# Kernel tuning notes

Measured on AMD Instinct MI355X. Metric: run time of the kernel, lower is better.

The kernel has to match this reference:

```python
import jax, jax.numpy as jnp
from jax import lax
import numpy as np

# ---- static config derived from init_kwargs ----
BATCH, SEQ, DM = 16, 1024, 512
EXPAND, DSTATE, DCONV, HEADDIM = 2, 64, 4, 64
DIN = EXPAND * DM                 # 1024 (d_inner)
NH = DIN // HEADDIM               # 16 heads
CONVDIM = DIN + 2 * DSTATE        # 1152 (x, B, C share depthwise conv)
DINPROJ = 2 * DIN + 2 * DSTATE + NH  # 2192
IN_CH, OUT_CH = SEQ, 1024         # Conv1d sees (B, L, d_model) as (N, C=L, len=d_model)
EPS = 1e-5


def setup_inputs() -> dict:
    key = jax.random.key(0)
    ks = jax.random.split(key, 8)
    sc = lambda k, shape, s=0.02: jax.random.normal(k, shape, jnp.float32) * s
    return {
        "x": jax.random.normal(ks[0], (BATCH, SEQ, DM), jnp.float32),
        # Mamba2 params (bias=False for in/out proj by default)
        "in_proj_w": sc(ks[1], (DINPROJ, DM)),
        "conv1d_w": sc(ks[2], (CONVDIM, DCONV), 0.1),   # depthwise kernel
        "conv1d_b": jnp.zeros((CONVDIM,), jnp.float32),
        "dt_bias": sc(ks[3], (NH,), 0.1),
        "A_log": jnp.log(jnp.linspace(1.0, 16.0, NH, dtype=jnp.float32)),
        "D": jnp.ones((NH,), jnp.float32),
        "rms_w": jnp.ones((DIN,), jnp.float32),
        "out_proj_w": sc(ks[4], (DM, DIN)),
        # trailing Conv1d(in_channels=SEQ, out_channels, k=3, pad=1)
        "conv_w": sc(ks[5], (OUT_CH, IN_CH, 3)),
        "conv_b": jnp.zeros((OUT_CH,), jnp.float32),
        # BatchNorm1d affine params (training-mode batch stats)
        "bn_gamma": jnp.ones((OUT_CH,), jnp.float32),
        "bn_beta": jnp.zeros((OUT_CH,), jnp.float32),
    }


def _mamba2(u, in_proj_w, conv1d_w, conv1d_b, dt_bias, A_log, D, rms_w, out_proj_w):
    B, L, _ = u.shape
    zxbcdt = u @ in_proj_w.T                          # (B, L, DINPROJ)
    z = zxbcdt[..., :DIN]
    xBC = zxbcdt[..., DIN:DIN + CONVDIM]
    dt = zxbcdt[..., DIN + CONVDIM:]                  # (B, L, NH)
    dt = jax.nn.softplus(dt + dt_bias)

    # causal depthwise conv over time + SiLU
    xBC_t = jnp.pad(xBC.transpose(0, 2, 1), ((0, 0), (0, 0), (DCONV - 1, 0)))
    xBC_c = lax.conv_general_dilated(
        xBC_t, conv1d_w[:, None, :], (1,), 'VALID',
        dimension_numbers=('NCH', 'OIH', 'NCH'), feature_group_count=CONVDIM)
    xBC = jax.nn.silu(xBC_c + conv1d_b[None, :, None]).transpose(0, 2, 1)  # (B, L, CONVDIM)

    x_in = xBC[..., :DIN].reshape(B, L, NH, HEADDIM)  # (B, L, H, P)
    Bm = xBC[..., DIN:DIN + DSTATE]                   # (B, L, N), ngroups=1
    Cm = xBC[..., DIN + DSTATE:]                      # (B, L, N)

    A = -jnp.exp(A_log)                               # (H,)
    dA = jnp.exp(dt * A)                              # (B, L, H)

    def step(h, inp):
        dA_t, dt_t, x_t, B_t, C_t = inp
        h = h * dA_t[:, :, None, None] + jnp.einsum('bh,bhp,bn->bhpn', dt_t, x_t, B_t)
        y_t = jnp.einsum('bhpn,bn->bhp', h, C_t)
        return h, y_t

    h0 = jnp.zeros((B, NH, HEADDIM, DSTATE), u.dtype)
    xs = (dA.transpose(1, 0, 2), dt.transpose(1, 0, 2),
          x_in.transpose(1, 0, 2, 3), Bm.transpose(1, 0, 2), Cm.transpose(1, 0, 2))
    _, ys = lax.scan(step, h0, xs)                    # (L, B, H, P)
    y = ys.transpose(1, 0, 2, 3) + D[None, None, :, None] * x_in
    y = y.reshape(B, L, DIN)

    # gated RMSNorm: norm(y * silu(z))
    y = y * jax.nn.silu(z)
    y = y * lax.rsqrt(jnp.mean(y * y, axis=-1, keepdims=True) + EPS) * rms_w
    return y @ out_proj_w.T                           # (B, L, DM)


def reference(x, in_proj_w, conv1d_w, conv1d_b, dt_bias, A_log, D, rms_w,
              out_proj_w, conv_w, conv_b, bn_gamma, bn_beta):
    u = _mamba2(x, in_proj_w, conv1d_w, conv1d_b, dt_bias, A_log, D, rms_w, out_proj_w)
    # Conv1d over (N, C=SEQ, len=DM), kernel 3, padding 1
    c = lax.conv_general_dilated(u, conv_w, (1,), [(1, 1)],
                                 dimension_numbers=('NCH', 'OIH', 'NCH'))
    c = c + conv_b[None, :, None]                     # (B, OUT_CH, DM)
    # BatchNorm1d (training-mode batch statistics, biased variance)
    mean = jnp.mean(c, axis=(0, 2), keepdims=True)
    var = jnp.mean((c - mean) ** 2, axis=(0, 2), keepdims=True)
    c = (c - mean) * lax.rsqrt(var + EPS)
    c = c * bn_gamma[None, :, None] + bn_beta[None, :, None]
    return jax.nn.silu(c)
```

## Files before the change

### kernel.cpp

```cpp
#include <hip/hip_runtime.h>
#include <hip/hip_bf16.h>

#define BATCH 16
#define SEQ   1024
#define DM    512
#define DSTATE 64
#define DIN   1024
#define NH    16
#define CONVDIM 1152
#define DINPROJ 2192
#define NPAD  2304
#define XDTW  1280
#define OC    1024
#define EPSF  1e-5f

typedef __attribute__((ext_vector_type(8))) short short8;
typedef __attribute__((ext_vector_type(4))) float f32x4;

__device__ __forceinline__ void g2lds16(const __hip_bfloat16* g, __hip_bfloat16* l) {
  __builtin_amdgcn_global_load_lds(
      (const __attribute__((address_space(1))) void*)g,
      (__attribute__((address_space(3))) void*)l, 16, 0, 0);
}

__device__ __forceinline__ float siluf(float x) { return x / (1.f + expf(-x)); }
__device__ __forceinline__ float b2f(unsigned short u) {
  return __uint_as_float(((unsigned int)u) << 16);
}
__device__ __forceinline__ unsigned short f2b(float v) {
  __hip_bfloat16 h = __float2bfloat16(v);
  return __builtin_bit_cast(unsigned short, h);
}

__global__ __launch_bounds__(256) void gemm1_kernel(
    const __hip_bfloat16* __restrict__ A,
    const __hip_bfloat16* __restrict__ B,
    __hip_bfloat16* __restrict__ zbuf,
    __hip_bfloat16* __restrict__ xdt)
{
  __shared__ __hip_bfloat16 sAB[2][2][8192];
  const int tid  = threadIdx.x;
  const int lane = tid & 63;
  const int wid  = tid >> 6;
  const int wr = wid >> 1, wc = wid & 1;
  const long row0 = (long)blockIdx.x * 128;
  const int  col0 = blockIdx.y * 128;
  const __hip_bfloat16* Ab = A + row0 * 512;
  const __hip_bfloat16* Bb = B + (long)col0 * 512;

  auto stage = [&](int kt, int buf) {
#pragma unroll
    for (int it = 0; it < 4; ++it) {
      int idx = it * 256 + tid;
      int r = idx >> 3;
      int kk = (idx & 7) << 3;
      g2lds16(Ab + (long)r * 512 + kt + kk, &sAB[buf][0][idx * 8]);
      g2lds16(Bb + (long)r * 512 + kt + kk, &sAB[buf][1][idx * 8]);
    }
  };

  f32x4 acc[4][4] = {};
  stage(0, 0);
  __syncthreads();
  int cur = 0;
  for (int kt = 0; kt < 512; kt += 64) {
    if (kt + 64 < 512) stage(kt + 64, cur ^ 1);
    const __hip_bfloat16* sA = &sAB[cur][0][0];
    const __hip_bfloat16* sB = &sAB[cur][1][0];
#pragma unroll
    for (int kk = 0; kk < 64; kk += 32) {
      const int kl = kk + (lane >> 4) * 8;
      short8 af[4], bfr[4];
#pragma unroll
      for (int m = 0; m < 4; ++m)
        af[m] = *(const short8*)(sA + (wr * 64 + m * 16 + (lane & 15)) * 64 + kl);
#pragma unroll
      for (int n = 0; n < 4; ++n)
        bfr[n] = *(const short8*)(sB + (wc * 64 + n * 16 + (lane & 15)) * 64 + kl);
#pragma unroll
      for (int m = 0; m < 4; ++m)
#pragma unroll
        for (int n = 0; n < 4; ++n)
          acc[m][n] = __builtin_amdgcn_mfma_f32_16x16x32_bf16(af[m], bfr[n], acc[m][n], 0, 0, 0);
    }
    __syncthreads();
    cur ^= 1;
  }

  __hip_bfloat16* Cb;
  int ldc, coff;
  if (col0 < 1024) { Cb = zbuf; ldc = 1024; coff = col0; }
  else             { Cb = xdt;  ldc = XDTW; coff = col0 - 1024; }
  const int rb = (int)row0 + wr * 64 + ((lane >> 4) << 2);
  const int cb = coff + wc * 64 + (lane & 15);
#pragma unroll
  for (int m = 0; m < 4; ++m)
#pragma unroll
    for (int n = 0; n < 4; ++n) {
      const int r = rb + m * 16, cc = cb + n * 16;
#pragma unroll
      for (int q = 0; q < 4; ++q)
        Cb[(long)(r + q) * ldc + cc] = __float2bfloat16(acc[m][n][q]);
    }
}

__global__ __launch_bounds__(256) void gemm2_trans_kernel(
    const __hip_bfloat16* __restrict__ A,
    const __hip_bfloat16* __restrict__ B,
    const float* __restrict__ rn,
    __hip_bfloat16* __restrict__ uTp)
{
  __shared__ unsigned short smem[2][2][8192];
  const int tid  = threadIdx.x;
  const int lane = tid & 63;
  const int wid  = tid >> 6;
  const int wr = wid >> 1, wc = wid & 1;
  const long row0 = (long)blockIdx.x * 128;
  const int  col0 = blockIdx.y * 128;
  const int  b  = (int)(row0 >> 10);
  const int  l0 = (int)(row0 & 1023);
  const __hip_bfloat16* Ab = A + row0 * 1024;
  const __hip_bfloat16* Bb = B + (long)col0 * 1024;

  auto stage = [&](int kt, int buf) {
#pragma unroll
    for (int it = 0; it < 4; ++it) {
      int idx = it * 256 + tid;
      int r = idx >> 3;
      int kk = (idx & 7) << 3;
      g2lds16(Ab + (long)r * 1024 + kt + kk, (__hip_bfloat16*)&smem[buf][0][idx * 8]);
      g2lds16(Bb + (long)r * 1024 + kt + kk, (__hip_bfloat16*)&smem[buf][1][idx * 8]);
    }
  };

  f32x4 acc[4][4] = {};
  stage(0, 0);
  __syncthreads();
  int cur = 0;
  for (int kt = 0; kt < 1024; kt += 64) {
    if (kt + 64 < 1024) stage(kt + 64, cur ^ 1);
    const __hip_bfloat16* sA = (const __hip_bfloat16*)&smem[cur][0][0];
    const __hip_bfloat16* sB = (const __hip_bfloat16*)&smem[cur][1][0];
#pragma unroll
    for (int kk = 0; kk < 64; kk += 32) {
      const int kl = kk + (lane >> 4) * 8;
      short8 af[4], bfr[4];
#pragma unroll
      for (int m = 0; m < 4; ++m)
        af[m] = *(const short8*)(sA + (wr * 64 + m * 16 + (lane & 15)) * 64 + kl);
#pragma unroll
      for (int n = 0; n < 4; ++n)
        bfr[n] = *(const short8*)(sB + (wc * 64 + n * 16 + (lane & 15)) * 64 + kl);
#pragma unroll
      for (int m = 0; m < 4; ++m)
#pragma unroll
        for (int n = 0; n < 4; ++n)
          acc[m][n] = __builtin_amdgcn_mfma_f32_16x16x32_bf16(af[m], bfr[n], acc[m][n], 0, 0, 0);
    }
    __syncthreads();
    cur ^= 1;
  }

  unsigned short* sT = &smem[0][0][0];
  const int rl = wr * 64 + ((lane >> 4) << 2);
  const int cl = wc * 64 + (lane & 15);
#pragma unroll
  for (int m = 0; m < 4; ++m) {
    float rnv[4];
#pragma unroll
    for (int q = 0; q < 4; ++q) rnv[q] = rn[row0 + rl + m * 16 + q];
#pragma unroll
    for (int n = 0; n < 4; ++n) {
      const int c = cl + n * 16;
#pragma unroll
      for (int q = 0; q < 4; ++q)
        sT[c * 128 + rl + m * 16 + q] = f2b(acc[m][n][q] * rnv[q]);
    }
  }
  __syncthreads();

  unsigned short* up = (unsigned short*)uTp + (long)b * 514 * 1024;
  const int w = tid >> 6;
#pragma unroll
  for (int k = 0; k < 32; ++k) {
    const int row = w * 32 + k;
    ushort2 o2;
    o2.x = sT[row * 128 + lane * 2];
    o2.y = sT[row * 128 + lane * 2 + 1];
    *(ushort2*)(up + (long)(col0 + row + 1) * 1024 + l0 + lane * 2) = o2;
  }
}

__global__ __launch_bounds__(256) void gemm_conv_kernel(
    const __hip_bfloat16* __restrict__ A,
    const __hip_bfloat16* __restrict__ uTp,
    float* __restrict__ C)
{
  const int f = blockIdx.x + 8 * (blockIdx.y + 4 * blockIdx.z);
  const int g = (f & 7) * 64 + (f >> 3);
  const int bx = g & 7, by = (g >> 3) & 3, bz = g >> 5;

  __shared__ __hip_bfloat16 sAB[2][2][8192];
  const int tid  = threadIdx.x;
  const int lane = tid & 63;
  const int wid  = tid >> 6;
  const int wr = wid >> 1, wc = wid & 1;
  const int row0 = bx * 128;
  const int col0 = by * 128;
  const __hip_bfloat16* Ab = A + (long)row0 * 3072;
  const __hip_bfloat16* Ub = uTp + (long)bz * 514 * 1024;

  auto stage = [&](int kt, int buf) {
    const int seg = kt >> 10;
    const int io  = kt & 1023;
#pragma unroll
    for (int it = 0; it < 4; ++it) {
      int idx = it * 256 + tid;
      int r = idx >> 3;
      int kk = (idx & 7) << 3;
      g2lds16(Ab + (long)r * 3072 + kt + kk, &sAB[buf][0][idx * 8]);
      g2lds16(Ub + (long)(col0 + r + seg) * 1024 + io + kk, &sAB[buf][1][idx * 8]);
    }
  };

  f32x4 acc[4][4] = {};
  stage(0, 0);
  __syncthreads();
  int cur = 0;
  for (int kt = 0; kt < 3072; kt += 64) {
    if (kt + 64 < 3072) stage(kt + 64, cur ^ 1);
    const __hip_bfloat16* sA = &sAB[cur][0][0];
    const __hip_bfloat16* sB = &sAB[cur][1][0];
#pragma unroll
    for (int kk = 0; kk < 64; kk += 32) {
      const int kl = kk + (lane >> 4) * 8;
      short8 af[4], bfr[4];
#pragma unroll
      for (int m = 0; m < 4; ++m)
        af[m] = *(const short8*)(sA + (wr * 64 + m * 16 + (lane & 15)) * 64 + kl);
#pragma unroll
      for (int n = 0; n < 4; ++n)
        bfr[n] = *(const short8*)(sB + (wc * 64 + n * 16 + (lane & 15)) * 64 + kl);
#pragma unroll
      for (int m = 0; m < 4; ++m)
#pragma unroll
        for (int n = 0; n < 4; ++n)
          acc[m][n] = __builtin_amdgcn_mfma_f32_16x16x32_bf16(af[m], bfr[n], acc[m][n], 0, 0, 0);
    }
    __syncthreads();
    cur ^= 1;
  }

  float* Cb = C + (long)bz * OC * DM;
  const int rb = row0 + wr * 64 + ((lane >> 4) << 2);
  const int cb = col0 + wc * 64 + (lane & 15);
#pragma unroll
  for (int m = 0; m < 4; ++m)
#pragma unroll
    for (int n = 0; n < 4; ++n) {
      const int r = rb + m * 16, cc = cb + n * 16;
#pragma unroll
      for (int q = 0; q < 4; ++q)
        Cb[(long)(r + q) * DM + cc] = acc[m][n][q];
    }
}

__global__ __launch_bounds__(256) void fill_kernel(float* __restrict__ out, float v, long n) {
  long i = (long)blockIdx.x * 256 + threadIdx.x;
  if (i < n) out[i] = v;
}

__global__ __launch_bounds__(256) void prep_kernel(
    const float* __restrict__ x, const float* __restrict__ w1,
    const float* __restrict__ w2, const float* __restrict__ rms_w,
    const float* __restrict__ w3,
    __hip_bfloat16* __restrict__ xbf, __hip_bfloat16* __restrict__ w1b,
    __hip_bfloat16* __restrict__ w2b, __hip_bfloat16* __restrict__ w3b)
{
  const int bid = blockIdx.x;
  if (bid < 8192) {
    long i = (long)bid * 256 + threadIdx.x;
    float4 v = *(const float4*)(x + i * 4);
    __hip_bfloat16* o = xbf + i * 4;
    o[0] = __float2bfloat16(v.x);
    o[1] = __float2bfloat16(v.y);
    o[2] = __float2bfloat16(v.z);
    o[3] = __float2bfloat16(v.w);
  } else if (bid < 12800) {
    int i = (bid - 8192) * 256 + threadIdx.x;
    int r = i >> 9;
    w1b[i] = (r < DINPROJ) ? __float2bfloat16(w1[i]) : __float2bfloat16(0.f);
  } else if (bid < 13312) {
    int i = (bid - 12800) * 256 + threadIdx.x;
    float4 v = *(const float4*)(w2 + (long)i * 4);
    float4 gw = *(const float4*)(rms_w + ((i * 4) & 1023));
    __hip_bfloat16* o = w2b + (long)i * 4;
    o[0] = __float2bfloat16(v.x * gw.x);
    o[1] = __float2bfloat16(v.y * gw.y);
    o[2] = __float2bfloat16(v.z * gw.z);
    o[3] = __float2bfloat16(v.w * gw.w);
  } else {
    int t = (bid - 13312) * 256 + threadIdx.x;
    int o = t >> 10, i = t & 1023;
    const float* p = w3 + (long)o * 3072 + i * 3;
    __hip_bfloat16* q = w3b + (long)o * 3072 + i;
    q[0]    = __float2bfloat16(p[0]);
    q[1024] = __float2bfloat16(p[1]);
    q[2048] = __float2bfloat16(p[2]);
  }
}

__global__ __launch_bounds__(256) void conv1d_slide_kernel(
    const __hip_bfloat16* __restrict__ xdt, const float* __restrict__ cw,
    const float* __restrict__ cb, const float* __restrict__ dt_bias,
    __hip_bfloat16* __restrict__ xbc, float* __restrict__ dtb)
{
  const int pair = blockIdx.x * 256 + threadIdx.x;
  const int c = pair * 2;
  if (c >= CONVDIM + NH) return;
  const int b  = blockIdx.z;
  const int l0 = blockIdx.y * 16;
  const long rowb = (long)b * SEQ;
  const unsigned short* src = (const unsigned short*)xdt + rowb * XDTW + c;

  if (c < CONVDIM) {
    const float4 wa = *(const float4*)(cw + c * 4);
    const float4 wb = *(const float4*)(cw + (c + 1) * 4);
    const float ba = cb[c], bb = cb[c + 1];
    float w0x, w0y, w1x, w1y, w2x, w2y;
    {
      ushort2 v;
      if (l0 >= 3) { v = *(const ushort2*)(src + (long)(l0 - 3) * XDTW); w0x = b2f(v.x); w0y = b2f(v.y); }
      else { w0x = 0.f; w0y = 0.f; }
      if (l0 >= 2) { v = *(const ushort2*)(src + (long)(l0 - 2) * XDTW); w1x = b2f(v.x); w1y = b2f(v.y); }
      else { w1x = 0.f; w1y = 0.f; }
      if (l0 >= 1) { v = *(const ushort2*)(src + (long)(l0 - 1) * XDTW); w2x = b2f(v.x); w2y = b2f(v.y); }
      else { w2x = 0.f; w2y = 0.f; }
    }
    unsigned short* dst = (unsigned short*)xbc + rowb * CONVDIM + c;
#pragma unroll
    for (int i = 0; i < 16; ++i) {
      const int l = l0 + i;
      const ushort2 v = *(const ushort2*)(src + (long)l * XDTW);
      const float xv0 = b2f(v.x), xv1 = b2f(v.y);
      float a0 = ba, a1 = bb;
      a0 += w0x * wa.x; a1 += w0y * wb.x;
      a0 += w1x * wa.y; a1 += w1y * wb.y;
      a0 += w2x * wa.z; a1 += w2y * wb.z;
      a0 += xv0 * wa.w; a1 += xv1 * wb.w;
      ushort2 o;
      o.x = f2b(siluf(a0));
      o.y = f2b(siluf(a1));
      *(ushort2*)(dst + (long)l * CONVDIM) = o;
      w0x = w1x; w0y = w1y; w1x = w2x; w1y = w2y; w2x = xv0; w2y = xv1;
    }
  } else {
    const int hh = c - CONVDIM;
    const float b0 = dt_bias[hh], b1 = dt_bias[hh + 1];
#pragma unroll
    for (int i = 0; i < 16; ++i) {
      const long l = l0 + i;
      const ushort2 v = *(const ushort2*)(src + l * XDTW);
      const float d0 = b2f(v.x) + b0, d1 = b2f(v.y) + b1;
      float2 o;
      o.x = fmaxf(d0, 0.f) + log1pf(expf(-fabsf(d0)));
      o.y = fmaxf(d1, 0.f) + log1pf(expf(-fabsf(d1)));
      *(float2*)(dtb + (rowb + l) * NH + hh) = o;
    }
  }
}

__global__ __launch_bounds__(256) void ssd_chunk_kernel(
    const __hip_bfloat16* __restrict__ xbc, const float* __restrict__ dtb,
    const float* __restrict__ A_log, __hip_bfloat16* __restrict__ ypre,
    __hip_bfloat16* __restrict__ Tbuf, float* __restrict__ Aprod)
{
  const int c = blockIdx.x, h = blockIdx.y, b = blockIdx.z;
  const int tid = threadIdx.x, lane = tid & 63, wid = tid >> 6;
  const int wr = wid >> 1, wc = wid & 1;
  const long r0 = (long)b * SEQ + c * 64;

  __shared__ unsigned short sB[64 * 72], sC[64 * 72], sXT[64 * 72],
                            sBwT[64 * 72], sM[64 * 72];
  __shared__ float sS[64], sDt[64];

  {
    const int j = tid >> 2, seg = (tid & 3) * 16;
    const unsigned short* row = (const unsigned short*)(xbc + (r0 + j) * CONVDIM);
    short8 v0 = *(const short8*)(row + DIN + seg);
    short8 v1 = *(const short8*)(row + DIN + seg + 8);
    *(short8*)&sB[j * 72 + seg] = v0;
    *(short8*)&sB[j * 72 + seg + 8] = v1;
    v0 = *(const short8*)(row + DIN + DSTATE + seg);
    v1 = *(const short8*)(row + DIN + DSTATE + seg + 8);
    *(short8*)&sC[j * 72 + seg] = v0;
    *(short8*)&sC[j * 72 + seg + 8] = v1;
    short8 x0 = *(const short8*)(row + h * 64 + seg);
    short8 x1 = *(const short8*)(row + h * 64 + seg + 8);
#pragma unroll
    for (int e = 0; e < 8; ++e) {
      sXT[(seg + e) * 72 + j] = (unsigned short)x0[e];
      sXT[(seg + 8 + e) * 72 + j] = (unsigned short)x1[e];
    }
  }
  if (tid < 64) {
    float dt = dtb[(r0 + tid) * NH + h];
    float s = -__expf(A_log[h]) * dt;
#pragma unroll
    for (int off = 1; off < 64; off <<= 1) {
      float o = __shfl_up(s, off);
      if (lane >= off) s += o;
    }
    sDt[tid] = dt;
    sS[tid] = s;
    if (tid == 63) Aprod[((b * 16 + h) * 16) + c] = __expf(s);
  }
  __syncthreads();

  {
    const int j = tid >> 2, n0 = (tid & 3) * 16;
    const float w = __expf(sS[63] - sS[j]) * sDt[j];
#pragma unroll
    for (int e = 0; e < 16; ++e)
      sBwT[(n0 + e) * 72 + j] = f2b(w * b2f(sB[j * 72 + n0 + e]));
  }
  {
    f32x4 acc1[2][2] = {};
#pragma unroll
    for (int kk = 0; kk < 64; kk += 32) {
      const int kl = kk + (lane >> 4) * 8;
      short8 af[2], bfr[2];
#pragma unroll
      for (int m = 0; m < 2; ++m)
        af[m] = *(const short8*)&sC[(wr * 32 + m * 16 + (lane & 15)) * 72 + kl];
#pragma unroll
      for (int n = 0; n < 2; ++n)
        bfr[n] = *(const short8*)&sB[(wc * 32 + n * 16 + (lane & 15)) * 72 + kl];
#pragma unroll
      for (int m = 0; m < 2; ++m)
#pragma unroll
        for (int n = 0; n < 2; ++n)
          acc1[m][n] = __builtin_amdgcn_mfma_f32_16x16x32_bf16(af[m], bfr[n], acc1[m][n], 0, 0, 0);
    }
    const int rq = (lane >> 4) * 4, cc = lane & 15;
#pragma unroll
    for (int m = 0; m < 2; ++m)
#pragma unroll
      for (int n = 0; n < 2; ++n)
#pragma unroll
        for (int q = 0; q < 4; ++q) {
          const int i = wr * 32 + m * 16 + rq + q;
          const int jj = wc * 32 + n * 16 + cc;
          float f = (jj <= i) ? __expf(sS[i] - sS[jj]) * sDt[jj] : 0.f;
          sM[i * 72 + jj] = f2b(acc1[m][n][q] * f);
        }
  }
  __syncthreads();

  f32x4 acc2[2][2] = {}, acc3[2][2] = {};
#pragma unroll
  for (int kk = 0; kk < 64; kk += 32) {
    const int kl = kk + (lane >> 4) * 8;
    short8 am[2], axB[2], axA[2], abw[2];
#pragma unroll
    for (int m = 0; m < 2; ++m) {
      am[m]  = *(const short8*)&sM[(wr * 32 + m * 16 + (lane & 15)) * 72 + kl];
      axA[m] = *(const short8*)&sXT[(wr * 32 + m * 16 + (lane & 15)) * 72 + kl];
    }
#pragma unroll
    for (int n = 0; n < 2; ++n) {
      axB[n] = *(const short8*)&sXT[(wc * 32 + n * 16 + (lane & 15)) * 72 + kl];
      abw[n] = *(const short8*)&sBwT[(wc * 32 + n * 16 + (lane & 15)) * 72 + kl];
    }
#pragma unroll
    for (int m = 0; m < 2; ++m)
#pragma unroll
      for (int n = 0; n < 2; ++n) {
        acc2[m][n] = __builtin_amdgcn_mfma_f32_16x16x32_bf16(am[m], axB[n], acc2[m][n], 0, 0, 0);
        acc3[m][n] = __builtin_amdgcn_mfma_f32_16x16x32_bf16(axA[m], abw[n], acc3[m][n], 0, 0, 0);
      }
  }
  const int rq = (lane >> 4) * 4, cc = lane & 15;
  const long tb = (((long)(b * 16 + h)) * 16 + c) * 4096;
#pragma unroll
  for (int m = 0; m < 2; ++m)
#pragma unroll
    for (int n = 0; n < 2; ++n)
#pragma unroll
      for (int q = 0; q < 4; ++q) {
        const int i = wr * 32 + m * 16 + rq + q;
        const int pj = wc * 32 + n * 16 + cc;
        ypre[(r0 + i) * DIN + h * 64 + pj] = __float2bfloat16(acc2[m][n][q]);
        Tbuf[tb + i * 64 + pj] = __float2bfloat16(acc3[m][n][q]);
      }
}

__global__ __launch_bounds__(1024) void ssd_state_kernel(
    __hip_bfloat16* __restrict__ Tbuf, const float* __restrict__ Aprod)
{
  const int bh = blockIdx.x;
  const int t = threadIdx.x;
  float h0 = 0.f, h1 = 0.f, h2 = 0.f, h3 = 0.f;
  unsigned short* base = (unsigned short*)Tbuf + (long)bh * 16 * 4096 + t * 4;
  for (int c = 0; c < 16; ++c) {
    unsigned short* p = base + (long)c * 4096;
    ushort4 tv = *(const ushort4*)p;
    ushort4 hv;
    hv.x = f2b(h0); hv.y = f2b(h1); hv.z = f2b(h2); hv.w = f2b(h3);
    *(ushort4*)p = hv;
    const float ap = Aprod[bh * 16 + c];
    h0 = h0 * ap + b2f(tv.x);
    h1 = h1 * ap + b2f(tv.y);
    h2 = h2 * ap + b2f(tv.z);
    h3 = h3 * ap + b2f(tv.w);
  }
}

__global__ __launch_bounds__(256) void ssd_out_kernel(
    const __hip_bfloat16* __restrict__ xbc, const float* __restrict__ dtb,
    const float* __restrict__ A_log, const __hip_bfloat16* __restrict__ Hbuf,
    const __hip_bfloat16* __restrict__ zbuf, const float* __restrict__ Dv,
    __hip_bfloat16* __restrict__ ypre)
{
  const int c = blockIdx.x, h = blockIdx.y, b = blockIdx.z;
  const int tid = threadIdx.x, lane = tid & 63, wid = tid >> 6;
  const int wr = wid >> 1, wc = wid & 1;
  const long r0 = (long)b * SEQ + c * 64;

  __shared__ unsigned short sC[64 * 72], sH[64 * 72];
  __shared__ float sS[64];

  {
    const int j = tid >> 2, seg = (tid & 3) * 16;
    const unsigned short* row = (const unsigned short*)(xbc + (r0 + j) * CONVDIM);
    short8 v0 = *(const short8*)(row + DIN + DSTATE + seg);
    short8 v1 = *(const short8*)(row + DIN + DSTATE + seg + 8);
    *(short8*)&sC[j * 72 + seg] = v0;
    *(short8*)&sC[j * 72 + seg + 8] = v1;
    const unsigned short* hrow =
        (const unsigned short*)Hbuf + (((long)(b * 16 + h)) * 16 + c) * 4096 + j * 64;
    v0 = *(const short8*)(hrow + seg);
    v1 = *(const short8*)(hrow + seg + 8);
    *(short8*)&sH[j * 72 + seg] = v0;
    *(short8*)&sH[j * 72 + seg + 8] = v1;
  }
  if (tid < 64) {
    float dt = dtb[(r0 + tid) * NH + h];
    float s = -__expf(A_log[h]) * dt;
#pragma unroll
    for (int off = 1; off < 64; off <<= 1) {
      float o = __shfl_up(s, off);
      if (lane >= off) s += o;
    }
    sS[tid] = s;
  }
  __syncthreads();

  f32x4 acc[2][2] = {};
#pragma unroll
  for (int kk = 0; kk < 64; kk += 32) {
    const int kl = kk + (lane >> 4) * 8;
    short8 af[2], bfr[2];
#pragma unroll
    for (int m = 0; m < 2; ++m)
      af[m] = *(const short8*)&sC[(wr * 32 + m * 16 + (lane & 15)) * 72 + kl];
#pragma unroll
    for (int n = 0; n < 2; ++n)
      bfr[n] = *(const short8*)&sH[(wc * 32 + n * 16 + (lane & 15)) * 72 + kl];
#pragma unroll
    for (int m = 0; m < 2; ++m)
#pragma unroll
      for (int n = 0; n < 2; ++n)
        acc[m][n] = __builtin_amdgcn_mfma_f32_16x16x32_bf16(af[m], bfr[n], acc[m][n], 0, 0, 0);
  }
  const float Dh = Dv[h];
  const int rq = (lane >> 4) * 4, cc = lane & 15;
#pragma unroll
  for (int m = 0; m < 2; ++m)
#pragma unroll
    for (int n = 0; n < 2; ++n)
#pragma unroll
      for (int q = 0; q < 4; ++q) {
        const int i = wr * 32 + m * 16 + rq + q;
        const int p = wc * 32 + n * 16 + cc;
        const long r = r0 + i;
        const long oidx = r * DIN + h * 64 + p;
        float yv = b2f(((const unsigned short*)ypre)[oidx]);
        float xv = b2f(((const unsigned short*)xbc)[r * CONVDIM + h * 64 + p]);
        float zv = b2f(((const unsigned short*)zbuf)[r * DIN + h * 64 + p]);
        yv += __expf(sS[i]) * acc[m][n][q] + Dh * xv;
        ypre[oidx] = __float2bfloat16(yv * siluf(zv));
      }
}

__global__ __launch_bounds__(256) void rmsn_kernel(const __hip_bfloat16* __restrict__ y,
                                                   float* __restrict__ rn)
{
  const long row = blockIdx.x;
  const int t = threadIdx.x;
  const ushort4 u = *(const ushort4*)((const unsigned short*)y + row * DIN + t * 4);
  float v0 = b2f(u.x), v1 = b2f(u.y), v2 = b2f(u.z), v3 = b2f(u.w);
  float ss = v0 * v0 + v1 * v1 + v2 * v2 + v3 * v3;
#pragma unroll
  for (int m = 32; m >= 1; m >>= 1) ss += __shfl_xor(ss, m);
  __shared__ float red[4];
  if ((t & 63) == 0) red[t >> 6] = ss;
  __syncthreads();
  if (t == 0) {
    ss = red[0] + red[1] + red[2] + red[3];
    rn[row] = rsqrtf(ss * (1.f / DIN) + EPSF);
  }
}

__global__ __launch_bounds__(256) void padzero_kernel(__hip_bfloat16* __restrict__ uTp) {
  int t = blockIdx.x * 256 + threadIdx.x;
  if (t >= 32768) return;
  int n = t >> 11, w = t & 2047;
  long row = (w >> 10) ? 513 : 0;
  uTp[(long)n * 514 * 1024 + row * 1024 + (w & 1023)] = __float2bfloat16(0.f);
}

__global__ __launch_bounds__(256) void bn_stats_kernel(const float* __restrict__ c,
                                                       float* __restrict__ stats)
{
  const int o = blockIdx.x, t = threadIdx.x;
  float s = 0.f, s2 = 0.f;
  for (int n = 0; n < BATCH; ++n) {
    const float* base = c + ((long)n * OC + o) * DM;
    for (int sp = t; sp < DM; sp += 256) { float v = base[sp]; s += v; s2 += v * v; }
  }
#pragma unroll
  for (int m = 32; m >= 1; m >>= 1) { s += __shfl_xor(s, m); s2 += __shfl_xor(s2, m); }
  __shared__ float r1[4], r2[4];
  if ((t & 63) == 0) { r1[t >> 6] = s; r2[t >> 6] = s2; }
  __syncthreads();
  if (t == 0) {
    s = r1[0] + r1[1] + r1[2] + r1[3];
    s2 = r2[0] + r2[1] + r2[2] + r2[3];
    float mean = s * (1.f / 8192.f);
    float var = s2 * (1.f / 8192.f) - mean * mean;
    stats[o] = mean;
    stats[OC + o] = rsqrtf(var + EPSF);
  }
}

__global__ __launch_bounds__(256) void bn_silu_kernel(const float* __restrict__ c,
    const float* __restrict__ stats, const float* __restrict__ gamma,
    const float* __restrict__ beta, float* __restrict__ out)
{
  long gid = (long)blockIdx.x * 256 + threadIdx.x;
  long base = gid * 4;
  int o = (int)((base >> 9) & (OC - 1));
  float mean = stats[o], rstd = stats[OC + o];
  float g = gamma[o] * rstd;
  float sh = beta[o] - mean * g;
  float4 v = *(const float4*)(c + base);
  float4 r;
  r.x = siluf(v.x * g + sh);
  r.y = siluf(v.y * g + sh);
  r.z = siluf(v.z * g + sh);
  r.w = siluf(v.w * g + sh);
  *(float4*)(out + base) = r;
}

extern "C" void kernel_launch(void* const* d_in, const int* in_sizes, int n_in,
                              void* d_out, int out_size, void* d_ws, size_t ws_size,
                              hipStream_t stream) {
  const float* x         = (const float*)d_in[0];
  const float* in_projw  = (const float*)d_in[1];
  const float* conv1dw   = (const float*)d_in[2];
  const float* conv1db   = (const float*)d_in[3];
  const float* dt_bias   = (const float*)d_in[4];
  const float* A_log     = (const float*)d_in[5];
  const float* Dv        = (const float*)d_in[6];
  const float* rms_w     = (const float*)d_in[7];
  const float* out_projw = (const float*)d_in[8];
  const float* conv_w    = (const float*)d_in[9];
  const float* bn_gamma  = (const float*)d_in[11];
  const float* bn_beta   = (const float*)d_in[12];
  float* out = (float*)d_out;
  char* ws = (char*)d_ws;

  __hip_bfloat16* zbuf = (__hip_bfloat16*)(ws + 0UL);
  __hip_bfloat16* xdt  = (__hip_bfloat16*)(ws + 33554432UL);
  __hip_bfloat16* xbcb = (__hip_bfloat16*)(ws + 75497472UL);
  __hip_bfloat16* ypb  = (__hip_bfloat16*)(ws + 113246208UL);
  __hip_bfloat16* xbf  = (__hip_bfloat16*)(ws + 146800640UL);
  __hip_bfloat16* w1b  = (__hip_bfloat16*)(ws + 163577856UL);
  __hip_bfloat16* w2b  = (__hip_bfloat16*)(ws + 165937152UL);
  __hip_bfloat16* w3b  = (__hip_bfloat16*)(ws + 166985728UL);
  float* dtb           = (float*)(ws + 173277184UL);
  float* Aprod         = (float*)(ws + 174325760UL);
  float* stats         = (float*)(ws + 174342144UL);
  float* rn            = (float*)(ws + 174350336UL);
  const size_t WS_NEED = 174415872UL;

  const long outn = (long)BATCH * OC * DM;
  if (ws_size < WS_NEED) {
    fill_kernel<<<(int)((outn + 255) / 256), 256, 0, stream>>>(out, (float)(ws_size >> 20), outn);
    return;
  }

  __hip_bfloat16* Tbuf = xdt;
  __hip_bfloat16* uTp  = xdt;
  float* cbuf = (float*)zbuf;

  prep_kernel<<<17408, 256, 0, stream>>>(x, in_projw, out_projw, rms_w, conv_w,
                                         xbf, w1b, w2b, w3b);

  gemm1_kernel<<<dim3(128, 18), 256, 0, stream>>>(xbf, w1b, zbuf, xdt);
  conv1d_slide_kernel<<<dim3(3, 64, BATCH), 256, 0, stream>>>(xdt, conv1dw, conv1db,
                                                              dt_bias, xbcb, dtb);
  ssd_chunk_kernel<<<dim3(16, 16, 16), 256, 0, stream>>>(xbcb, dtb, A_log, ypb, Tbuf, Aprod);
  ssd_state_kernel<<<256, 1024, 0, stream>>>(Tbuf, Aprod);
  ssd_out_kernel<<<dim3(16, 16, 16), 256, 0, stream>>>(xbcb, dtb, A_log, Tbuf, zbuf, Dv, ypb);
  rmsn_kernel<<<16384, 256, 0, stream>>>(ypb, rn);
  padzero_kernel<<<128, 256, 0, stream>>>(uTp);
  gemm2_trans_kernel<<<dim3(128, 4), 256, 0, stream>>>(ypb, w2b, rn, uTp);
  gemm_conv_kernel<<<dim3(8, 4, 16), 256, 0, stream>>>(w3b, uTp, cbuf);
  bn_stats_kernel<<<1024, 256, 0, stream>>>(cbuf, stats);
  bn_silu_kernel<<<8192, 256, 0, stream>>>(cbuf, stats, bn_gamma, bn_beta, out);
}
```

Baseline: 299.1 us.

## Fuse RMSNorm sum-of-squares into SSD output and store conv result as bf16

The RMSNorm sum of squares is now accumulated inside ssd_out_kernel through shared-memory and global atomics, so the separate rmsn_kernel no longer re-reads the whole gated activation. Padding zeroing and the rsqrt finalisation are merged into one small kernel, and the accumulator is cleared in prep_kernel. The conv GEMM output is written as bf16 instead of fp32, which halves the traffic for bn_stats and bn_silu. The cost is extra atomics and lower precision in the pre-BatchNorm values, and the global float atomic sum is order-dependent.

```diff
diff --git a/kernel.cpp b/kernel.cpp
--- a/kernel.cpp
+++ b/kernel.cpp
@@ -194,7 +194,7 @@
 __global__ __launch_bounds__(256) void gemm_conv_kernel(
     const __hip_bfloat16* __restrict__ A,
     const __hip_bfloat16* __restrict__ uTp,
-    float* __restrict__ C)
+    __hip_bfloat16* __restrict__ C)
 {
   const int f = blockIdx.x + 8 * (blockIdx.y + 4 * blockIdx.z);
   const int g = (f & 7) * 64 + (f >> 3);
@@ -251,7 +251,7 @@
     cur ^= 1;
   }
 
-  float* Cb = C + (long)bz * OC * DM;
+  __hip_bfloat16* Cb = C + (long)bz * OC * DM;
   const int rb = row0 + wr * 64 + ((lane >> 4) << 2);
   const int cb = col0 + wc * 64 + (lane & 15);
 #pragma unroll
@@ -261,7 +261,7 @@
       const int r = rb + m * 16, cc = cb + n * 16;
 #pragma unroll
       for (int q = 0; q < 4; ++q)
-        Cb[(long)(r + q) * DM + cc] = acc[m][n][q];
+        Cb[(long)(r + q) * DM + cc] = __float2bfloat16(acc[m][n][q]);
     }
 }
 
@@ -275,7 +275,8 @@
     const float* __restrict__ w2, const float* __restrict__ rms_w,
     const float* __restrict__ w3,
     __hip_bfloat16* __restrict__ xbf, __hip_bfloat16* __restrict__ w1b,
-    __hip_bfloat16* __restrict__ w2b, __hip_bfloat16* __restrict__ w3b)
+    __hip_bfloat16* __restrict__ w2b, __hip_bfloat16* __restrict__ w3b,
+    float* __restrict__ rnacc)
 {
   const int bid = blockIdx.x;
   if (bid < 8192) {
@@ -299,7 +300,7 @@
     o[1] = __float2bfloat16(v.y * gw.y);
     o[2] = __float2bfloat16(v.z * gw.z);
     o[3] = __float2bfloat16(v.w * gw.w);
-  } else {
+  } else if (bid < 17408) {
     int t = (bid - 13312) * 256 + threadIdx.x;
     int o = t >> 10, i = t & 1023;
     const float* p = w3 + (long)o * 3072 + i * 3;
@@ -307,6 +308,9 @@
     q[0]    = __float2bfloat16(p[0]);
     q[1024] = __float2bfloat16(p[1]);
     q[2048] = __float2bfloat16(p[2]);
+  } else {
+    int i = (bid - 17408) * 256 + threadIdx.x;
+    rnacc[i] = 0.f;
   }
 }
 
@@ -520,7 +524,7 @@
     const __hip_bfloat16* __restrict__ xbc, const float* __restrict__ dtb,
     const float* __restrict__ A_log, const __hip_bfloat16* __restrict__ Hbuf,
     const __hip_bfloat16* __restrict__ zbuf, const float* __restrict__ Dv,
-    __hip_bfloat16* __restrict__ ypre)
+    __hip_bfloat16* __restrict__ ypre, float* __restrict__ rnacc)
 {
   const int c = blockIdx.x, h = blockIdx.y, b = blockIdx.z;
   const int tid = threadIdx.x, lane = tid & 63, wid = tid >> 6;
@@ -529,6 +533,7 @@
 
   __shared__ unsigned short sC[64 * 72], sH[64 * 72];
   __shared__ float sS[64];
+  __shared__ float sRed[64];
 
   {
     const int j = tid >> 2, seg = (tid & 3) * 16;
@@ -545,6 +550,7 @@
     *(short8*)&sH[j * 72 + seg + 8] = v1;
   }
   if (tid < 64) {
+    sRed[tid] = 0.f;
     float dt = dtb[(r0 + tid) * NH + h];
     float s = -__expf(A_log[h]) * dt;
 #pragma unroll
@@ -575,6 +581,7 @@
   }
   const float Dh = Dv[h];
   const int rq = (lane >> 4) * 4, cc = lane & 15;
+  float rsum[2][4] = {};
 #pragma unroll
   for (int m = 0; m < 2; ++m)
 #pragma unroll
@@ -589,45 +596,46 @@
         float xv = b2f(((const unsigned short*)xbc)[r * CONVDIM + h * 64 + p]);
         float zv = b2f(((const unsigned short*)zbuf)[r * DIN + h * 64 + p]);
         yv += __expf(sS[i]) * acc[m][n][q] + Dh * xv;
-        ypre[oidx] = __float2bfloat16(yv * siluf(zv));
+        const float g = yv * siluf(zv);
+        rsum[m][q] += g * g;
+        ypre[oidx] = __float2bfloat16(g);
       }
-}
-
-__global__ __launch_bounds__(256) void rmsn_kernel(const __hip_bfloat16* __restrict__ y,
-                                                   float* __restrict__ rn)
-{
-  const long row = blockIdx.x;
-  const int t = threadIdx.x;
-  const ushort4 u = *(const ushort4*)((const unsigned short*)y + row * DIN + t * 4);
-  float v0 = b2f(u.x), v1 = b2f(u.y), v2 = b2f(u.z), v3 = b2f(u.w);
-  float ss = v0 * v0 + v1 * v1 + v2 * v2 + v3 * v3;
-#pragma unroll
-  for (int m = 32; m >= 1; m >>= 1) ss += __shfl_xor(ss, m);
-  __shared__ float red[4];
-  if ((t & 63) == 0) red[t >> 6] = ss;
-  __syncthreads();
-  if (t == 0) {
-    ss = red[0] + red[1] + red[2] + red[3];
-    rn[row] = rsqrtf(ss * (1.f / DIN) + EPSF);
-  }
-}
-
-__global__ __launch_bounds__(256) void padzero_kernel(__hip_bfloat16* __restrict__ uTp) {
-  int t = blockIdx.x * 256 + threadIdx.x;
-  if (t >= 32768) return;
-  int n = t >> 11, w = t & 2047;
-  long row = (w >> 10) ? 513 : 0;
-  uTp[(long)n * 514 * 1024 + row * 1024 + (w & 1023)] = __float2bfloat16(0.f);
-}
-
-__global__ __launch_bounds__(256) void bn_stats_kernel(const float* __restrict__ c,
-                                                       float* __restrict__ stats)
+#pragma unroll
+  for (int m = 0; m < 2; ++m)
+#pragma unroll
+    for (int q = 0; q < 4; ++q)
+      atomicAdd(&sRed[wr * 32 + m * 16 + rq + q], rsum[m][q]);
+  __syncthreads();
+  if (tid < 64) atomicAdd(&rnacc[r0 + tid], sRed[tid]);
+}
+
+__global__ __launch_bounds__(256) void rnfin_pad_kernel(
+    const float* __restrict__ rnacc, float* __restrict__ rn,
+    __hip_bfloat16* __restrict__ uTp)
+{
+  const int bid = blockIdx.x;
+  if (bid < 64) {
+    int i = bid * 256 + threadIdx.x;
+    rn[i] = rsqrtf(rnacc[i] * (1.f / DIN) + EPSF);
+  } else {
+    int t = (bid - 64) * 256 + threadIdx.x;
+    int n = t >> 11, w = t & 2047;
+    long row = (w >> 10) ? 513 : 0;
+    uTp[(long)n * 514 * 1024 + row * 1024 + (w & 1023)] = __float2bfloat16(0.f);
+  }
+}
+
+__global__ __launch_bounds__(256) void bn_stats_kernel(
+    const __hip_bfloat16* __restrict__ c, float* __restrict__ stats)
 {
   const int o = blockIdx.x, t = threadIdx.x;
   float s = 0.f, s2 = 0.f;
   for (int n = 0; n < BATCH; ++n) {
-    const float* base = c + ((long)n * OC + o) * DM;
-    for (int sp = t; sp < DM; sp += 256) { float v = base[sp]; s += v; s2 += v * v; }
+    const unsigned short* base = (const unsigned short*)c + ((long)n * OC + o) * DM;
+    ushort2 v = *(const ushort2*)(base + t * 2);
+    float a = b2f(v.x), bb = b2f(v.y);
+    s += a + bb;
+    s2 += a * a + bb * bb;
   }
 #pragma unroll
   for (int m = 32; m >= 1; m >>= 1) { s += __shfl_xor(s, m); s2 += __shfl_xor(s2, m); }
@@ -644,9 +652,10 @@
   }
 }
 
-__global__ __launch_bounds__(256) void bn_silu_kernel(const float* __restrict__ c,
-    const float* __restrict__ stats, const float* __restrict__ gamma,
-    const float* __restrict__ beta, float* __restrict__ out)
+__global__ __launch_bounds__(256) void bn_silu_kernel(
+    const __hip_bfloat16* __restrict__ c, const float* __restrict__ stats,
+    const float* __restrict__ gamma, const float* __restrict__ beta,
+    float* __restrict__ out)
 {
   long gid = (long)blockIdx.x * 256 + threadIdx.x;
   long base = gid * 4;
@@ -654,12 +663,12 @@
   float mean = stats[o], rstd = stats[OC + o];
   float g = gamma[o] * rstd;
   float sh = beta[o] - mean * g;
-  float4 v = *(const float4*)(c + base);
+  ushort4 v = *(const ushort4*)((const unsigned short*)c + base);
   float4 r;
-  r.x = siluf(v.x * g + sh);
-  r.y = siluf(v.y * g + sh);
-  r.z = siluf(v.z * g + sh);
-  r.w = siluf(v.w * g + sh);
+  r.x = siluf(b2f(v.x) * g + sh);
+  r.y = siluf(b2f(v.y) * g + sh);
+  r.z = siluf(b2f(v.z) * g + sh);
+  r.w = siluf(b2f(v.w) * g + sh);
   *(float4*)(out + base) = r;
 }
 
@@ -693,7 +702,8 @@
   float* Aprod         = (float*)(ws + 174325760UL);
   float* stats         = (float*)(ws + 174342144UL);
   float* rn            = (float*)(ws + 174350336UL);
-  const size_t WS_NEED = 174415872UL;
+  float* rnacc         = (float*)(ws + 174415872UL);
+  const size_t WS_NEED = 174481408UL;
 
   const long outn = (long)BATCH * OC * DM;
   if (ws_size < WS_NEED) {
@@ -703,19 +713,19 @@
 
   __hip_bfloat16* Tbuf = xdt;
   __hip_bfloat16* uTp  = xdt;
-  float* cbuf = (float*)zbuf;
-
-  prep_kernel<<<17408, 256, 0, stream>>>(x, in_projw, out_projw, rms_w, conv_w,
-                                         xbf, w1b, w2b, w3b);
+  __hip_bfloat16* cbuf = zbuf;
+
+  prep_kernel<<<17472, 256, 0, stream>>>(x, in_projw, out_projw, rms_w, conv_w,
+                                         xbf, w1b, w2b, w3b, rnacc);
 
   gemm1_kernel<<<dim3(128, 18), 256, 0, stream>>>(xbf, w1b, zbuf, xdt);
   conv1d_slide_kernel<<<dim3(3, 64, BATCH), 256, 0, stream>>>(xdt, conv1dw, conv1db,
                                                               dt_bias, xbcb, dtb);
   ssd_chunk_kernel<<<dim3(16, 16, 16), 256, 0, stream>>>(xbcb, dtb, A_log, ypb, Tbuf, Aprod);
   ssd_state_kernel<<<256, 1024, 0, stream>>>(Tbuf, Aprod);
-  ssd_out_kernel<<<dim3(16, 16, 16), 256, 0, stream>>>(xbcb, dtb, A_log, Tbuf, zbuf, Dv, ypb);
-  rmsn_kernel<<<16384, 256, 0, stream>>>(ypb, rn);
-  padzero_kernel<<<128, 256, 0, stream>>>(uTp);
+  ssd_out_kernel<<<dim3(16, 16, 16), 256, 0, stream>>>(xbcb, dtb, A_log, Tbuf, zbuf,
+                                                       Dv, ypb, rnacc);
+  rnfin_pad_kernel<<<192, 256, 0, stream>>>(rnacc, rn, uTp);
   gemm2_trans_kernel<<<dim3(128, 4), 256, 0, stream>>>(ypb, w2b, rn, uTp);
   gemm_conv_kernel<<<dim3(8, 4, 16), 256, 0, stream>>>(w3b, uTp, cbuf);
   bn_stats_kernel<<<1024, 256, 0, stream>>>(cbuf, stats);
```

Measured after the change: 329.6 us. 1.1x slower.
